# Performance work log

Measured on AMD Instinct MI355X. Metric: run time of the kernel, lower is better.

Reference implementation:

```python
import jax, jax.numpy as jnp
import numpy as np

EPS = 1e-5  # BatchNorm1d default eps


def _xavier_uniform(key, shape):
    # torch xavier: fan_in = shape[1]*prod(shape[2:]), fan_out = shape[0]*prod(shape[2:])
    rf = int(np.prod(shape[2:])) if len(shape) > 2 else 1
    fan_in = shape[1] * rf
    fan_out = shape[0] * rf
    bound = float(np.sqrt(6.0 / (fan_in + fan_out)))
    return jax.random.uniform(key, shape, jnp.float32, -bound, bound)


def setup_inputs() -> dict:
    key = jax.random.key(0)
    ks = jax.random.split(key, 6)
    d_in, h1, h2, d_out = 256, 512, 512, 256
    B = 4096
    x = jax.random.normal(ks[0], (B, 1, d_in), dtype=jnp.float32)
    W1 = _xavier_uniform(ks[1], (h1, d_in))
    b1 = jnp.zeros((h1,), jnp.float32)
    gamma = jnp.ones((1, 1, 1), jnp.float32)   # BatchNorm1d(1) weight
    beta = jnp.zeros((1, 1, 1), jnp.float32)   # BatchNorm1d(1) bias
    coeffs2 = _xavier_uniform(ks[2], (2, h2, h1, 16))
    bias2 = jnp.zeros((1, h2), jnp.float32)
    coeffs3 = _xavier_uniform(ks[3], (2, d_out, h2, 8))
    bias3 = jnp.zeros((1, d_out), jnp.float32)
    return {"x": x, "W1": W1, "b1": b1, "gamma": gamma, "beta": beta,
            "coeffs2": coeffs2, "bias2": bias2, "coeffs3": coeffs3, "bias3": bias3}


def _fourier_kan(x, coeffs, bias, gridsize):
    # x: (N, in)  coeffs: (2, out, in, grid)  ->  (N, out)
    k = jnp.arange(1, gridsize + 1, dtype=x.dtype)          # (grid,)
    arg = x[:, :, None] * k                                  # (N, in, grid) -- basis computed ONCE
    y = jnp.einsum('nig,oig->no', jnp.cos(arg), coeffs[0])
    y = y + jnp.einsum('nig,oig->no', jnp.sin(arg), coeffs[1])
    return y + bias


def reference(x, W1, b1, gamma, beta, coeffs2, bias2, coeffs3, bias3):
    # x: (B, 1, d_in)
    h = jnp.einsum('bcd,hd->bch', x, W1) + b1                # Linear -> (B,1,h1)
    # BatchNorm1d(1), training-mode batch stats over (N, L) for the single channel
    mean = jnp.mean(h, axis=(0, 2), keepdims=True)
    var = jnp.mean((h - mean) ** 2, axis=(0, 2), keepdims=True)
    h = gamma * (h - mean) * jax.lax.rsqrt(var + EPS) + beta
    h = jax.nn.relu(h)
    h = h.reshape(-1, h.shape[-1])                           # (B, h1)
    h = _fourier_kan(h, coeffs2, bias2, 16)                  # (B, h2)
    h = _fourier_kan(h, coeffs3, bias3, 8)                   # (B, out)
    return jax.nn.softmax(h, axis=1)
```

## Files before the change

### kernel.cpp

```cpp
#include <hip/hip_runtime.h>
#include <hip/hip_fp16.h>
#include <stdint.h>

typedef unsigned short u16;
typedef unsigned int u32;
typedef long i64;
typedef short bf16x8 __attribute__((ext_vector_type(8)));
typedef float f32x4 __attribute__((ext_vector_type(4)));

#define SCALE_C   1024.f
#define INV_SCALE 0.0009765625f

__device__ __forceinline__ float bf2f(u16 v) { return __uint_as_float(((u32)v) << 16); }

__device__ __forceinline__ u16 f2bf(float a) {
  u32 u = __float_as_uint(a); u += 0x7FFFu + ((u >> 16) & 1u); return (u16)(u >> 16);
}

__device__ __forceinline__ u32 packbf2(float a, float b) {
  u32 ua = __float_as_uint(a); ua += 0x7FFFu + ((ua >> 16) & 1u);
  u32 ub = __float_as_uint(b); ub += 0x7FFFu + ((ub >> 16) & 1u);
  return (ua >> 16) | (ub & 0xFFFF0000u);
}

__device__ __forceinline__ u32 packfp8x4(float a, float b, float c, float d) {
  u32 lo = (u32)__builtin_amdgcn_cvt_pk_fp8_f32(a, b, 0, false);
  return (u32)__builtin_amdgcn_cvt_pk_fp8_f32(c, d, (int)lo, true);
}

__device__ __forceinline__ float inval(const void* p, int idx, int isf) {
  return isf ? ((const float*)p)[idx] : bf2f(((const u16*)p)[idx]);
}

__device__ __forceinline__ void async_cp16(const void* g, void* l) {
  __builtin_amdgcn_global_load_lds(
      (const __attribute__((address_space(1))) void*)g,
      (__attribute__((address_space(3))) void*)l, 16, 0, 0);
}

__device__ __forceinline__ void basis16(float a, u32* pk) {
  float s1, c1; __sincosf(a, &s1, &c1);
  float t2 = c1 + c1;
  float cg[16], sg[16];
  cg[0] = c1; sg[0] = s1;
  cg[1] = fmaf(t2, c1, -1.f); sg[1] = t2 * s1;
  #pragma unroll
  for (int g = 2; g < 16; ++g) {
    cg[g] = fmaf(t2, cg[g-1], -cg[g-2]);
    sg[g] = fmaf(t2, sg[g-1], -sg[g-2]);
  }
  #pragma unroll
  for (int j = 0; j < 4; ++j) pk[j]   = packfp8x4(cg[4*j], cg[4*j+1], cg[4*j+2], cg[4*j+3]);
  #pragma unroll
  for (int j = 0; j < 4; ++j) pk[4+j] = packfp8x4(sg[4*j], sg[4*j+1], sg[4*j+2], sg[4*j+3]);
}

__device__ __forceinline__ void split_body(
    const void* __restrict__ src, u16* __restrict__ dst, int i, int isf, int lo_pos)
{
  int row = i >> 6, g = i & 63;
  float v[4];
  if (isf) {
    float4 t = ((const float4*)src)[i];
    v[0] = t.x; v[1] = t.y; v[2] = t.z; v[3] = t.w;
  } else {
    uint2 t = ((const uint2*)src)[i];
    const u16* p = (const u16*)&t;
    v[0] = bf2f(p[0]); v[1] = bf2f(p[1]); v[2] = bf2f(p[2]); v[3] = bf2f(p[3]);
  }
  u16 hi[4]; float lo[4];
  #pragma unroll
  for (int j = 0; j < 4; ++j) { hi[j] = f2bf(v[j]); lo[j] = v[j] - bf2f(hi[j]); }
  u32 hw0 = (u32)hi[0] | ((u32)hi[1] << 16);
  u32 hw1 = (u32)hi[2] | ((u32)hi[3] << 16);
  u32 lw0 = packbf2(lo[0], lo[1]);
  u32 lw1 = packbf2(lo[2], lo[3]);
  u32* base = (u32*)(dst + (size_t)row * 768);
  int c = g * 2;
  base[c] = hw0; base[c + 1] = hw1;
  if (lo_pos == 1) {
    base[128 + c] = lw0; base[128 + c + 1] = lw1;
    base[256 + c] = hw0; base[256 + c + 1] = hw1;
  } else {
    base[128 + c] = hw0; base[128 + c + 1] = hw1;
    base[256 + c] = lw0; base[256 + c + 1] = lw1;
  }
}

__global__ __launch_bounds__(256) void prep_all_kernel(
    const void* __restrict__ x, const void* __restrict__ W1,
    u16* __restrict__ Xs, u16* __restrict__ W1s,
    const void* __restrict__ c2, unsigned char* __restrict__ w2f8,
    const void* __restrict__ c3, unsigned char* __restrict__ w3f8,
    int* __restrict__ flag)
{
  __shared__ int sf[4];
  const int t = threadIdx.x, wave = t >> 6;
  {
    float v = fabsf(bf2f(((const u16*)W1)[t & 127]));
    int bad = !(v < 1e6f);
    unsigned long long b = __ballot(bad);
    if ((t & 63) == 0) sf[wave] = (b != 0ull) ? 1 : 0;
  }
  __syncthreads();
  const int isf = sf[0] | sf[1] | sf[2] | sf[3];
  const int bid = blockIdx.x;
  if (bid == 0 && t == 0) *flag = isf;
  if (bid < 1024) {
    split_body(x, Xs, bid * 256 + t, isf, 1);
  } else if (bid < 1152) {
    split_body(W1, W1s, (bid - 1024) * 256 + t, isf, 2);
  } else if (bid < 2176) {
    int u = (bid - 1152) * 256 + t;
    int o = u >> 9, i = u & 511;
    u32* d = (u32*)(w2f8 + (size_t)o * 16384 + i * 32);
    if (isf) {
      const float4* f0 = (const float4*)((const float*)c2 + ((size_t)o * 512 + i) * 16);
      const float4* f1 = (const float4*)((const float*)c2 + (size_t)512 * 512 * 16 + ((size_t)o * 512 + i) * 16);
      #pragma unroll
      for (int j = 0; j < 4; ++j) { float4 v = f0[j]; d[j]   = packfp8x4(v.x*SCALE_C, v.y*SCALE_C, v.z*SCALE_C, v.w*SCALE_C); }
      #pragma unroll
      for (int j = 0; j < 4; ++j) { float4 v = f1[j]; d[4+j] = packfp8x4(v.x*SCALE_C, v.y*SCALE_C, v.z*SCALE_C, v.w*SCALE_C); }
    } else {
      const u16* s0 = (const u16*)c2 + ((size_t)o * 512 + i) * 16;
      const u16* s1 = (const u16*)c2 + (size_t)512 * 512 * 16 + ((size_t)o * 512 + i) * 16;
      #pragma unroll
      for (int j = 0; j < 4; ++j) d[j]   = packfp8x4(bf2f(s0[4*j])*SCALE_C, bf2f(s0[4*j+1])*SCALE_C, bf2f(s0[4*j+2])*SCALE_C, bf2f(s0[4*j+3])*SCALE_C);
      #pragma unroll
      for (int j = 0; j < 4; ++j) d[4+j] = packfp8x4(bf2f(s1[4*j])*SCALE_C, bf2f(s1[4*j+1])*SCALE_C, bf2f(s1[4*j+2])*SCALE_C, bf2f(s1[4*j+3])*SCALE_C);
    }
  } else {
    int u = (bid - 2176) * 256 + t;
    int o = u >> 9, i = u & 511;
    u32* d = (u32*)(w3f8 + (size_t)o * 8192 + i * 16);
    if (isf) {
      const float4* f0 = (const float4*)((const float*)c3 + ((size_t)o * 512 + i) * 8);
      const float4* f1 = (const float4*)((const float*)c3 + (size_t)256 * 512 * 8 + ((size_t)o * 512 + i) * 8);
      #pragma unroll
      for (int j = 0; j < 2; ++j) { float4 v = f0[j]; d[j]   = packfp8x4(v.x*SCALE_C, v.y*SCALE_C, v.z*SCALE_C, v.w*SCALE_C); }
      #pragma unroll
      for (int j = 0; j < 2; ++j) { float4 v = f1[j]; d[2+j] = packfp8x4(v.x*SCALE_C, v.y*SCALE_C, v.z*SCALE_C, v.w*SCALE_C); }
    } else {
      const u16* s0 = (const u16*)c3 + ((size_t)o * 512 + i) * 8;
      const u16* s1 = (const u16*)c3 + (size_t)256 * 512 * 8 + ((size_t)o * 512 + i) * 8;
      #pragma unroll
      for (int j = 0; j < 2; ++j) d[j]   = packfp8x4(bf2f(s0[4*j])*SCALE_C, bf2f(s0[4*j+1])*SCALE_C, bf2f(s0[4*j+2])*SCALE_C, bf2f(s0[4*j+3])*SCALE_C);
      #pragma unroll
      for (int j = 0; j < 2; ++j) d[2+j] = packfp8x4(bf2f(s1[4*j])*SCALE_C, bf2f(s1[4*j+1])*SCALE_C, bf2f(s1[4*j+2])*SCALE_C, bf2f(s1[4*j+3])*SCALE_C);
    }
  }
}

#define L1_LD 136
__global__ __launch_bounds__(256) void l1_kernel(
    const u16* __restrict__ xs, const u16* __restrict__ w1s, const void* __restrict__ b1,
    const int* __restrict__ flag, float* __restrict__ H, float2* __restrict__ PT)
{
  __shared__ u16 sA[64 * L1_LD];
  __shared__ u16 sB[64 * L1_LD];
  __shared__ float redbuf[8];
  const int n0 = blockIdx.x * 64, o0 = blockIdx.y * 64;
  const int t = threadIdx.x, wave = t >> 6, lane = t & 63, quad = lane >> 4, l16 = lane & 15;
  const int isf = *flag;
  f32x4 acc[4] = {};
  for (int ks = 0; ks < 768; ks += 128) {
    #pragma unroll
    for (int r = 0; r < 4; ++r) {
      int idx = t + r * 256, row = idx >> 4, col = idx & 15;
      *(uint4*)&sA[row * L1_LD + col * 8] =
          *((const uint4*)(xs + (size_t)(n0 + row) * 768 + ks) + col);
    }
    #pragma unroll
    for (int r = 0; r < 4; ++r) {
      int idx = t + r * 256, row = idx >> 4, col = idx & 15;
      *(uint4*)&sB[row * L1_LD + col * 8] =
          *((const uint4*)(w1s + (size_t)(o0 + row) * 768 + ks) + col);
    }
    __syncthreads();
    #pragma unroll
    for (int kk = 0; kk < 128; kk += 32) {
      bf16x8 av = *(const bf16x8*)&sA[(wave * 16 + l16) * L1_LD + kk + quad * 8];
      #pragma unroll
      for (int fo = 0; fo < 4; ++fo) {
        bf16x8 bv = *(const bf16x8*)&sB[(fo * 16 + l16) * L1_LD + kk + quad * 8];
        acc[fo] = __builtin_amdgcn_mfma_f32_16x16x32_bf16(av, bv, acc[fo], 0, 0, 0);
      }
    }
    __syncthreads();
  }
  float s = 0.f, sq = 0.f;
  #pragma unroll
  for (int fo = 0; fo < 4; ++fo) {
    int o = o0 + fo * 16 + l16;
    float bias = inval(b1, o, isf);
    #pragma unroll
    for (int r = 0; r < 4; ++r) {
      int n = n0 + wave * 16 + quad * 4 + r;
      float h = acc[fo][r] + bias;
      H[(size_t)n * 512 + o] = h;
      s += h; sq += h * h;
    }
  }
  #pragma unroll
  for (int off = 32; off; off >>= 1) { s += __shfl_down(s, off); sq += __shfl_down(sq, off); }
  if (lane == 0) { redbuf[wave] = s; redbuf[4 + wave] = sq; }
  __syncthreads();
  if (t == 0) {
    float S = redbuf[0] + redbuf[1] + redbuf[2] + redbuf[3];
    float Q = redbuf[4] + redbuf[5] + redbuf[6] + redbuf[7];
    PT[blockIdx.y * 64 + blockIdx.x] = make_float2(S, Q);
  }
}

#define K2_LDB 128
__global__ __launch_bounds__(512, 4) void kan2_kernel(
    const float* __restrict__ H, const unsigned char* __restrict__ w2f8,
    const void* __restrict__ gammap, const void* __restrict__ betap,
    const int* __restrict__ flag, const float2* __restrict__ PT,
    float* __restrict__ P, int kzT)
{
  __shared__ __attribute__((aligned(16))) unsigned char smem[65536];
  __shared__ float sred[8];
  const int n0 = blockIdx.x * 128, o0 = blockIdx.y * 128, kz = blockIdx.z;
  const int t = threadIdx.x, wave = t >> 6, lane = t & 63, quad = lane >> 4, l16 = lane & 15;
  const int nst = 128 / kzT;
  const int i0 = kz * nst * 4;
  const int csw = (l16 & 7) << 4;
  const int isf = *flag;

  const int pt = t - 256;
  const int am = (pt >> 1) & 127;
  const int ib = (pt & 1) * 2;
  const int r0 = (pt >> 3) & 31, seg = pt & 7;
  const unsigned char* bsrc = w2f8 + (size_t)(o0 + r0) * 16384 + (size_t)i0 * 32
                              + ((seg * 16) ^ ((r0 & 7) << 4));
  const float* hsrc = H + (size_t)(n0 + am) * 512 + i0 + ib;
  const int asw = (am & 7) << 4;
  float mean = 0.f, gs = 0.f, beta = 0.f;
  float2 ph2 = make_float2(0.f, 0.f);
  u32 pk0[8], pk1[8];

  if (wave >= 4) {
    unsigned char* b0 = smem + 32768 + (wave - 4) * 1024;
    #pragma unroll
    for (int p = 0; p < 4; ++p)
      async_cp16(bsrc + (size_t)p * 32 * 16384, b0 + p * 4096);
    float2 pa = PT[pt], pb = PT[pt + 256];
    float ss = pa.x + pb.x, qs = pa.y + pb.y;
    #pragma unroll
    for (int off = 32; off; off >>= 1) { ss += __shfl_down(ss, off); qs += __shfl_down(qs, off); }
    if (lane == 0) { sred[(wave - 4) * 2] = ss; sred[(wave - 4) * 2 + 1] = qs; }
  }
  __syncthreads();
  if (wave >= 4) {
    const float Ssum = sred[0] + sred[2] + sred[4] + sred[6];
    const float Qsum = sred[1] + sred[3] + sred[5] + sred[7];
    const float Nn = 4096.f * 512.f;
    mean = Ssum / Nn;
    const float rstd = rsqrtf(Qsum / Nn - mean * mean + 1e-5f);
    gs = inval(gammap, 0, isf) * rstd;
    beta = inval(betap, 0, isf);
    ph2 = *(const float2*)hsrc; hsrc += 4;
    float a0 = fmaxf((ph2.x - mean) * gs + beta, 0.f);
    float a1 = fmaxf((ph2.y - mean) * gs + beta, 0.f);
    basis16(a0, pk0);
    basis16(a1, pk1);
    *(uint4*)&smem[am * K2_LDB + ((ib * 32) ^ asw)]           = *(uint4*)&pk0[0];
    *(uint4*)&smem[am * K2_LDB + ((ib * 32 + 16) ^ asw)]      = *(uint4*)&pk0[4];
    *(uint4*)&smem[am * K2_LDB + (((ib + 1) * 32) ^ asw)]     = *(uint4*)&pk1[0];
    *(uint4*)&smem[am * K2_LDB + (((ib + 1) * 32 + 16) ^ asw)] = *(uint4*)&pk1[4];
    if (nst > 1) { ph2 = *(const float2*)hsrc; hsrc += 4; }
  }
  __syncthreads();

  f32x4 acc[2][8] = {};
  const int wm = wave * 32;
  int cur = 0;
  for (int s = 0; s < nst; ++s) {
    const int nxt = cur ^ 1;
    if (wave >= 4) {
      if (s + 1 < nst) {
        bsrc += 128;
        unsigned char* bn = smem + 32768 + nxt * 16384 + (wave - 4) * 1024;
        #pragma unroll
        for (int p = 0; p < 4; ++p)
          async_cp16(bsrc + (size_t)p * 32 * 16384, bn + p * 4096);
        float a0 = fmaxf((ph2.x - mean) * gs + beta, 0.f);
        float a1 = fmaxf((ph2.y - mean) * gs + beta, 0.f);
        basis16(a0, pk0);
        basis16(a1, pk1);
        unsigned char* an = smem + nxt * 16384;
        *(uint4*)&an[am * K2_LDB + ((ib * 32) ^ asw)]            = *(uint4*)&pk0[0];
        *(uint4*)&an[am * K2_LDB + ((ib * 32 + 16) ^ asw)]       = *(uint4*)&pk0[4];
        *(uint4*)&an[am * K2_LDB + (((ib + 1) * 32) ^ asw)]      = *(uint4*)&pk1[0];
        *(uint4*)&an[am * K2_LDB + (((ib + 1) * 32 + 16) ^ asw)] = *(uint4*)&pk1[4];
        if (s + 2 < nst) { ph2 = *(const float2*)hsrc; hsrc += 4; }
      }
    } else {
      const unsigned char* ac = smem + cur * 16384;
      const unsigned char* bc = smem + 32768 + cur * 16384;
      #pragma unroll
      for (int kk = 0; kk < 128; kk += 32) {
        const int cb = (kk + quad * 8) ^ csw;
        i64 bfr[8], afr[2];
        #pragma unroll
        for (int fo = 0; fo < 8; ++fo)
          bfr[fo] = *(const i64*)&bc[(fo * 16 + l16) * K2_LDB + cb];
        #pragma unroll
        for (int fm = 0; fm < 2; ++fm)
          afr[fm] = *(const i64*)&ac[(wm + fm * 16 + l16) * K2_LDB + cb];
        #pragma unroll
        for (int fm = 0; fm < 2; ++fm)
        #pragma unroll
        for (int fo = 0; fo < 8; ++fo)
          acc[fm][fo] = __builtin_amdgcn_mfma_f32_16x16x32_fp8_fp8(afr[fm], bfr[fo], acc[fm][fo], 0, 0, 0);
      }
    }
    __syncthreads();
    cur = nxt;
  }
  if (wave < 4) {
    float* Pk = P + (size_t)kz * (4096 * 512);
    #pragma unroll
    for (int fm = 0; fm < 2; ++fm)
    #pragma unroll
    for (int fo = 0; fo < 8; ++fo) {
      int o = o0 + fo * 16 + l16;
      #pragma unroll
      for (int r = 0; r < 4; ++r) {
        int n = n0 + wm + fm * 16 + quad * 4 + r;
        Pk[(size_t)n * 512 + o] = acc[fm][fo][r] * INV_SCALE;
      }
    }
  }
}

#define K3_LDB 128
__global__ __launch_bounds__(256) void kan3_kernel(
    const float* __restrict__ P2, const void* __restrict__ bias2,
    const unsigned char* __restrict__ w3f8,
    const int* __restrict__ flag, float* __restrict__ Q, int kzT2)
{
  __shared__ unsigned char sA8[32 * K3_LDB];
  __shared__ unsigned char sB8[256 * K3_LDB];
  const int n0 = blockIdx.x * 32, kz = blockIdx.z;
  const int t = threadIdx.x, wave = t >> 6, lane = t & 63, quad = lane >> 4, l16 = lane & 15;
  const int wo = wave * 64;
  const int am = t >> 3, ai = t & 7;
  const int nst = 10 + (kz < 4 ? 1 : 0);
  const int i0 = (kz * 10 + (kz < 4 ? kz : 4)) * 8;
  const int r0 = t >> 3, seg = t & 7;
  const int isf = *flag;
  const unsigned char* bsrc = w3f8 + (size_t)r0 * 8192 + (size_t)i0 * 16
                              + ((seg * 16) ^ ((r0 & 7) << 4));
  const float* psrc = P2 + (size_t)(n0 + am) * 512 + i0 + ai;
  unsigned char* ldsB = &sB8[wave * 8 * K3_LDB];
  const int acol = (ai * 16) ^ ((am & 7) << 4);
  const int csw  = (l16 & 7) << 4;
  f32x4 acc[2][4] = {};
  #pragma unroll
  for (int p = 0; p < 8; ++p)
    async_cp16(bsrc + (size_t)p * 32 * 8192, ldsB + p * 32 * K3_LDB);
  float ph;
  {
    float v = inval(bias2, i0 + ai, isf);
    for (int k = 0; k < kzT2; ++k) v += psrc[(size_t)k * 4096 * 512];
    ph = v;
  }
  for (int s = 0; s < nst; ++s) {
    {
      float s1, c1; __sincosf(ph, &s1, &c1);
      float t2 = c1 + c1;
      float cg[8], sg[8];
      cg[0] = c1; sg[0] = s1;
      cg[1] = fmaf(t2, c1, -1.f); sg[1] = t2 * s1;
      #pragma unroll
      for (int g = 2; g < 8; ++g) {
        cg[g] = fmaf(t2, cg[g-1], -cg[g-2]);
        sg[g] = fmaf(t2, sg[g-1], -sg[g-2]);
      }
      u32 pk[4];
      pk[0] = packfp8x4(cg[0], cg[1], cg[2], cg[3]);
      pk[1] = packfp8x4(cg[4], cg[5], cg[6], cg[7]);
      pk[2] = packfp8x4(sg[0], sg[1], sg[2], sg[3]);
      pk[3] = packfp8x4(sg[4], sg[5], sg[6], sg[7]);
      *(uint4*)&sA8[am * K3_LDB + acol] = *(uint4*)&pk[0];
    }
    __syncthreads();
    psrc += 8;
    if (s + 1 < nst) {
      float v = inval(bias2, i0 + (s + 1) * 8 + ai, isf);
      for (int k = 0; k < kzT2; ++k) v += psrc[(size_t)k * 4096 * 512];
      ph = v;
    }
    #pragma unroll
    for (int kk = 0; kk < 128; kk += 32) {
      const int cb = (kk + quad * 8) ^ csw;
      i64 bfr[4], afr[2];
      #pragma unroll
      for (int fo = 0; fo < 4; ++fo)
        bfr[fo] = *(const i64*)&sB8[(wo + fo * 16 + l16) * K3_LDB + cb];
      #pragma unroll
      for (int fm = 0; fm < 2; ++fm)
        afr[fm] = *(const i64*)&sA8[(fm * 16 + l16) * K3_LDB + cb];
      #pragma unroll
      for (int fm = 0; fm < 2; ++fm)
      #pragma unroll
      for (int fo = 0; fo < 4; ++fo)
        acc[fm][fo] = __builtin_amdgcn_mfma_f32_16x16x32_fp8_fp8(afr[fm], bfr[fo], acc[fm][fo], 0, 0, 0);
    }
    __syncthreads();
    bsrc += 128;
    if (s + 1 < nst) {
      #pragma unroll
      for (int p = 0; p < 8; ++p)
        async_cp16(bsrc + (size_t)p * 32 * 8192, ldsB + p * 32 * K3_LDB);
    }
  }
  float* Qk = Q + (size_t)kz * (4096 * 256);
  #pragma unroll
  for (int fm = 0; fm < 2; ++fm)
  #pragma unroll
  for (int fo = 0; fo < 4; ++fo) {
    int o = wo + fo * 16 + l16;
    #pragma unroll
    for (int r = 0; r < 4; ++r) {
      int n = n0 + fm * 16 + quad * 4 + r;
      Qk[(size_t)n * 256 + o] = acc[fm][fo][r] * INV_SCALE;
    }
  }
}

__global__ __launch_bounds__(256) void softmax_kernel(
    const float* __restrict__ Q, const void* __restrict__ bias3,
    const int* __restrict__ flag, float* __restrict__ out)
{
  const int t = threadIdx.x, wave = t >> 6, lane = t & 63;
  const int row = blockIdx.x * 4 + wave;
  const int isf = *flag;
  size_t base = (size_t)row * 256 + lane * 4;
  float v0 = 0.f, v1 = 0.f, v2 = 0.f, v3 = 0.f;
  #pragma unroll
  for (int k = 0; k < 6; ++k) {
    float4 a = *(const float4*)(Q + (size_t)k * 4096 * 256 + base);
    v0 += a.x; v1 += a.y; v2 += a.z; v3 += a.w;
  }
  int o = lane * 4;
  v0 += inval(bias3, o + 0, isf);
  v1 += inval(bias3, o + 1, isf);
  v2 += inval(bias3, o + 2, isf);
  v3 += inval(bias3, o + 3, isf);
  float m = fmaxf(fmaxf(v0, v1), fmaxf(v2, v3));
  #pragma unroll
  for (int off = 32; off; off >>= 1) m = fmaxf(m, __shfl_xor(m, off));
  float e0 = __expf(v0 - m), e1 = __expf(v1 - m), e2 = __expf(v2 - m), e3 = __expf(v3 - m);
  float s = e0 + e1 + e2 + e3;
  #pragma unroll
  for (int off = 32; off; off >>= 1) s += __shfl_xor(s, off);
  float inv = 1.f / s;
  *(float4*)(out + base) = make_float4(e0 * inv, e1 * inv, e2 * inv, e3 * inv);
}

extern "C" void kernel_launch(void* const* d_in, const int* in_sizes, int n_in,
                              void* d_out, int out_size, void* d_ws, size_t ws_size,
                              hipStream_t stream)
{
  const void* x     = d_in[0];
  const void* W1    = d_in[1];
  const void* b1    = d_in[2];
  const void* gamma = d_in[3];
  const void* beta  = d_in[4];
  const void* c2    = d_in[5];
  const void* bias2 = d_in[6];
  const void* c3    = d_in[7];
  const void* bias3 = d_in[8];

  const int kz2 = 4;

  char* ws = (char*)d_ws;
  float*          H    = (float*)(ws + 0);
  unsigned char*  W2F8 = (unsigned char*)(ws + (16ull << 20));
  unsigned char*  W3F8 = (unsigned char*)(ws + (24ull << 20));
  u16*            Xs   = (u16*)(ws + (26ull << 20));
  u16*            W1s  = (u16*)(ws + (33ull << 20));
  float*          P2   = (float*)(ws + (34ull << 20));
  float*          Q3   = (float*)(ws + 0);
  size_t tail = (34ull << 20) + (size_t)kz2 * (8ull << 20) + 524288;
  float2* PT   = (float2*)(ws + tail);
  int*    FLAG = (int*)   (ws + tail + 65536);

  prep_all_kernel<<<dim3(2688), dim3(256), 0, stream>>>(x, W1, Xs, W1s, c2, W2F8, c3, W3F8, FLAG);
  l1_kernel   <<<dim3(64, 8), dim3(256), 0, stream>>>(Xs, W1s, b1, FLAG, H, PT);
  kan2_kernel <<<dim3(32, 4, kz2), dim3(512), 0, stream>>>(H, W2F8, gamma, beta, FLAG, PT, P2, kz2);
  kan3_kernel <<<dim3(128, 1, 6), dim3(256), 0, stream>>>(P2, bias2, W3F8, FLAG, Q3, kz2);
  softmax_kernel<<<dim3(1024), dim3(256), 0, stream>>>(Q3, bias3, FLAG, (float*)d_out);
}
```

Before: 200.2 us.

## Permute FP8 K-layout so MFMA operand loads use 128-bit LDS reads

Changes the packed FP8 layout of the layer-2 coefficients and the on-the-fly basis tiles so that, within each 128-wide K slab, each lane's two consecutive 32-wide MFMA K-chunks sit in 16 contiguous bytes. The consumer waves then fetch A and B fragments with 128-bit LDS reads instead of 64-bit ones, halving LDS read instructions, and raise wave priority around the MFMA block. Because the same permutation of K is applied to both operands, the dot products are unchanged, but the preprocessing store pattern becomes 8-byte scattered writes.

```diff
diff --git a/kernel.cpp b/kernel.cpp
--- a/kernel.cpp
+++ b/kernel.cpp
@@ -7,6 +7,7 @@
 typedef long i64;
 typedef short bf16x8 __attribute__((ext_vector_type(8)));
 typedef float f32x4 __attribute__((ext_vector_type(4)));
+typedef long i64x2 __attribute__((ext_vector_type(2)));
 
 #define SCALE_C   1024.f
 #define INV_SCALE 0.0009765625f
@@ -113,21 +114,28 @@
   } else if (bid < 2176) {
     int u = (bid - 1152) * 256 + t;
     int o = u >> 9, i = u & 511;
-    u32* d = (u32*)(w2f8 + (size_t)o * 16384 + i * 32);
+    u32 pk[8];
     if (isf) {
       const float4* f0 = (const float4*)((const float*)c2 + ((size_t)o * 512 + i) * 16);
       const float4* f1 = (const float4*)((const float*)c2 + (size_t)512 * 512 * 16 + ((size_t)o * 512 + i) * 16);
       #pragma unroll
-      for (int j = 0; j < 4; ++j) { float4 v = f0[j]; d[j]   = packfp8x4(v.x*SCALE_C, v.y*SCALE_C, v.z*SCALE_C, v.w*SCALE_C); }
-      #pragma unroll
-      for (int j = 0; j < 4; ++j) { float4 v = f1[j]; d[4+j] = packfp8x4(v.x*SCALE_C, v.y*SCALE_C, v.z*SCALE_C, v.w*SCALE_C); }
+      for (int j = 0; j < 4; ++j) { float4 v = f0[j]; pk[j]   = packfp8x4(v.x*SCALE_C, v.y*SCALE_C, v.z*SCALE_C, v.w*SCALE_C); }
+      #pragma unroll
+      for (int j = 0; j < 4; ++j) { float4 v = f1[j]; pk[4+j] = packfp8x4(v.x*SCALE_C, v.y*SCALE_C, v.z*SCALE_C, v.w*SCALE_C); }
     } else {
       const u16* s0 = (const u16*)c2 + ((size_t)o * 512 + i) * 16;
       const u16* s1 = (const u16*)c2 + (size_t)512 * 512 * 16 + ((size_t)o * 512 + i) * 16;
       #pragma unroll
-      for (int j = 0; j < 4; ++j) d[j]   = packfp8x4(bf2f(s0[4*j])*SCALE_C, bf2f(s0[4*j+1])*SCALE_C, bf2f(s0[4*j+2])*SCALE_C, bf2f(s0[4*j+3])*SCALE_C);
-      #pragma unroll
-      for (int j = 0; j < 4; ++j) d[4+j] = packfp8x4(bf2f(s1[4*j])*SCALE_C, bf2f(s1[4*j+1])*SCALE_C, bf2f(s1[4*j+2])*SCALE_C, bf2f(s1[4*j+3])*SCALE_C);
+      for (int j = 0; j < 4; ++j) pk[j]   = packfp8x4(bf2f(s0[4*j])*SCALE_C, bf2f(s0[4*j+1])*SCALE_C, bf2f(s0[4*j+2])*SCALE_C, bf2f(s0[4*j+3])*SCALE_C);
+      #pragma unroll
+      for (int j = 0; j < 4; ++j) pk[4+j] = packfp8x4(bf2f(s1[4*j])*SCALE_C, bf2f(s1[4*j+1])*SCALE_C, bf2f(s1[4*j+2])*SCALE_C, bf2f(s1[4*j+3])*SCALE_C);
+    }
+    uint2* b128 = (uint2*)(w2f8 + (size_t)o * 16384 + (size_t)(i & ~3) * 32);
+    const int il = i & 3;
+    #pragma unroll
+    for (int j2 = 0; j2 < 4; ++j2) {
+      uint2 v; v.x = pk[2*j2]; v.y = pk[2*j2+1];
+      b128[j2 * 4 + il] = v;
     }
   } else {
     int u = (bid - 2176) * 256 + t;
@@ -265,10 +273,11 @@
     float a1 = fmaxf((ph2.y - mean) * gs + beta, 0.f);
     basis16(a0, pk0);
     basis16(a1, pk1);
-    *(uint4*)&smem[am * K2_LDB + ((ib * 32) ^ asw)]           = *(uint4*)&pk0[0];
-    *(uint4*)&smem[am * K2_LDB + ((ib * 32 + 16) ^ asw)]      = *(uint4*)&pk0[4];
-    *(uint4*)&smem[am * K2_LDB + (((ib + 1) * 32) ^ asw)]     = *(uint4*)&pk1[0];
-    *(uint4*)&smem[am * K2_LDB + (((ib + 1) * 32 + 16) ^ asw)] = *(uint4*)&pk1[4];
+    #pragma unroll
+    for (int j2 = 0; j2 < 4; ++j2) {
+      u32 v[4] = { pk0[2*j2], pk0[2*j2+1], pk1[2*j2], pk1[2*j2+1] };
+      *(uint4*)&smem[am * K2_LDB + ((j2 * 32 + ib * 8) ^ asw)] = *(uint4*)v;
+    }
     if (nst > 1) { ph2 = *(const float2*)hsrc; hsrc += 4; }
   }
   __syncthreads();
@@ -290,31 +299,41 @@
         basis16(a0, pk0);
         basis16(a1, pk1);
         unsigned char* an = smem + nxt * 16384;
-        *(uint4*)&an[am * K2_LDB + ((ib * 32) ^ asw)]            = *(uint4*)&pk0[0];
-        *(uint4*)&an[am * K2_LDB + ((ib * 32 + 16) ^ asw)]       = *(uint4*)&pk0[4];
-        *(uint4*)&an[am * K2_LDB + (((ib + 1) * 32) ^ asw)]      = *(uint4*)&pk1[0];
-        *(uint4*)&an[am * K2_LDB + (((ib + 1) * 32 + 16) ^ asw)] = *(uint4*)&pk1[4];
+        #pragma unroll
+        for (int j2 = 0; j2 < 4; ++j2) {
+          u32 v[4] = { pk0[2*j2], pk0[2*j2+1], pk1[2*j2], pk1[2*j2+1] };
+          *(uint4*)&an[am * K2_LDB + ((j2 * 32 + ib * 8) ^ asw)] = *(uint4*)v;
+        }
         if (s + 2 < nst) { ph2 = *(const float2*)hsrc; hsrc += 4; }
       }
     } else {
       const unsigned char* ac = smem + cur * 16384;
       const unsigned char* bc = smem + 32768 + cur * 16384;
-      #pragma unroll
-      for (int kk = 0; kk < 128; kk += 32) {
-        const int cb = (kk + quad * 8) ^ csw;
-        i64 bfr[8], afr[2];
+      __builtin_amdgcn_s_setprio(1);
+      #pragma unroll
+      for (int h = 0; h < 2; ++h) {
+        const int cb = (quad * 32 + 16 * h) ^ csw;
+        i64x2 aq0 = *(const i64x2*)&ac[(wm + l16) * K2_LDB + cb];
+        i64x2 aq1 = *(const i64x2*)&ac[(wm + 16 + l16) * K2_LDB + cb];
         #pragma unroll
-        for (int fo = 0; fo < 8; ++fo)
-          bfr[fo] = *(const i64*)&bc[(fo * 16 + l16) * K2_LDB + cb];
-        #pragma unroll
-        for (int fm = 0; fm < 2; ++fm)
-          afr[fm] = *(const i64*)&ac[(wm + fm * 16 + l16) * K2_LDB + cb];
-        #pragma unroll
-        for (int fm = 0; fm < 2; ++fm)
-        #pragma unroll
-        for (int fo = 0; fo < 8; ++fo)
-          acc[fm][fo] = __builtin_amdgcn_mfma_f32_16x16x32_fp8_fp8(afr[fm], bfr[fo], acc[fm][fo], 0, 0, 0);
+        for (int g = 0; g < 2; ++g) {
+          i64x2 bq[4];
+          #pragma unroll
+          for (int j = 0; j < 4; ++j)
+            bq[j] = *(const i64x2*)&bc[((g * 4 + j) * 16 + l16) * K2_LDB + cb];
+          #pragma unroll
+          for (int j = 0; j < 4; ++j) {
+            acc[0][g*4+j] = __builtin_amdgcn_mfma_f32_16x16x32_fp8_fp8(aq0[0], bq[j][0], acc[0][g*4+j], 0, 0, 0);
+            acc[1][g*4+j] = __builtin_amdgcn_mfma_f32_16x16x32_fp8_fp8(aq1[0], bq[j][0], acc[1][g*4+j], 0, 0, 0);
+          }
+          #pragma unroll
+          for (int j = 0; j < 4; ++j) {
+            acc[0][g*4+j] = __builtin_amdgcn_mfma_f32_16x16x32_fp8_fp8(aq0[1], bq[j][1], acc[0][g*4+j], 0, 0, 0);
+            acc[1][g*4+j] = __builtin_amdgcn_mfma_f32_16x16x32_fp8_fp8(aq1[1], bq[j][1], acc[1][g*4+j], 0, 0, 0);
+          }
+        }
       }
+      __builtin_amdgcn_s_setprio(0);
     }
     __syncthreads();
     cur = nxt;
```

Result: no change. 200.6 us (+0.2%).
